# Performance work log

Hardware: AMD Instinct MI355X
Metric: run time of the kernel (lower is better)

Reference implementation:

```python
import jax, jax.numpy as jnp
import numpy as np

N_CH = 128      # n_channels (out_channels)
MID = 128       # mid_channels
NF = 16         # num_filters
N_NODES = 50000


def _omeg():
    i = jnp.arange(NF, dtype=jnp.float32)
    return (10.0 * N_CH ** (1.0 - 2.0 * i / NF)).reshape(1, NF)


def setup_inputs() -> dict:
    key = jax.random.key(0)
    ks = jax.random.split(key, 16)
    E = 800000
    inp = {
        "x": jax.random.normal(ks[0], (N_NODES, N_CH), jnp.float32),
        "edge_index": jax.random.randint(ks[1], (2, E), 0, N_NODES, jnp.int64),
        "edge_attr": jax.random.normal(ks[2], (E, N_CH), jnp.float32),
        "x_pos": jax.random.normal(ks[3], (N_NODES, 3), jnp.float32),
    }
    def lin(k, fan_in, fan_out):
        kw, kb = jax.random.split(k)
        bound = 1.0 / np.sqrt(fan_in)
        w = jax.random.uniform(kw, (fan_in, fan_out), jnp.float32, -bound, bound)
        b = jax.random.uniform(kb, (fan_out,), jnp.float32, -bound, bound)
        return w, b
    inp["w1"], inp["b1"] = lin(ks[4], N_CH, N_CH)          # atomwise1
    inp["mw1"], inp["mb1"] = lin(ks[5], 2 * NF + 2 * N_CH, MID)  # message MLP
    inp["mw2"], inp["mb2"] = lin(ks[6], MID, MID)
    inp["mw3"], inp["mb3"] = lin(ks[7], MID, N_CH)
    inp["w2"], inp["b2"] = lin(ks[8], N_CH, N_CH)          # atomwise2
    inp["w3"], inp["b3"] = lin(ks[9], N_CH, N_CH)          # atomwise3
    return inp


def reference(x, edge_index, edge_attr, x_pos, w1, b1, mw1, mb1, mw2, mb2, mw3, mb3, w2, b2, w3, b3):
    h = x @ w1 + b1                                   # atomwise1 [N, C]
    src, dst = edge_index[0], edge_index[1]           # PyG: x_j = src, x_i = dst
    r = jnp.linalg.norm(x_pos[dst] - x_pos[src], axis=-1, keepdims=True)  # [E,1], p=2
    feat = r * _omeg()                                # [E, NF]
    msg_in = jnp.concatenate([jnp.sin(feat), jnp.cos(feat), edge_attr, h[src]], axis=-1)
    m = jax.nn.gelu(msg_in @ mw1 + mb1, approximate=False)
    m = jax.nn.gelu(m @ mw2 + mb2, approximate=False)
    m = m @ mw3 + mb3                                 # dropout is identity at eval
    agg = jax.ops.segment_sum(m, dst, num_segments=N_NODES)
    h = h + agg                                       # residual in cfconv
    out = jax.nn.relu(h @ w2 + b2) @ w3 + b3
    return out
```

## Files before the change

### kernel.cpp

```cpp
#include <hip/hip_runtime.h>
#include <math.h>

#define NCH 128
#define TE 64
#define TF 32
#define AP 296
#define AF 132
#define WP 40
#define XP 136

typedef __attribute__((ext_vector_type(8))) _Float16 half8;
typedef __attribute__((ext_vector_type(4))) _Float16 half4;
typedef __attribute__((ext_vector_type(4))) float f32x4;

__device__ __forceinline__ float gelu_exact(float v) {
    return 0.5f * v * (1.0f + erff(v * 0.70710678118654752f));
}

__device__ __forceinline__ float erf_fast(float x) {
    float ax = fabsf(x);
    float t  = __builtin_amdgcn_rcpf(fmaf(0.3275911f, ax, 1.0f));
    float p  = fmaf(t, 1.061405429f, -1.453152027f);
    p = fmaf(t, p, 1.421413741f);
    p = fmaf(t, p, -0.284496736f);
    p = fmaf(t, p, 0.254829592f);
    float e  = exp2f(-ax * ax * 1.4426950408889634f);
    float r  = fmaf(-p * t, e, 1.0f);
    return copysignf(r, x);
}

__device__ __forceinline__ float gelu_fast(float v) {
    return 0.5f * v * (1.0f + erf_fast(v * 0.70710678118654752f));
}

__device__ __forceinline__ void sincos_rev(float rev, float* s, float* c) {
    float fr = rev - floorf(rev);
#if __has_builtin(__builtin_amdgcn_sinf) && __has_builtin(__builtin_amdgcn_cosf)
    *s = __builtin_amdgcn_sinf(fr);
    *c = __builtin_amdgcn_cosf(fr);
#else
    float rad = fr * 6.283185307179586f;
    *s = sinf(rad);
    *c = cosf(rad);
#endif
}

__global__ __launch_bounds__(256) void k_hist(const int* __restrict__ ei,
                                              int* __restrict__ cnt, int E) {
    int e = blockIdx.x * 256 + threadIdx.x;
    if (e < E) atomicAdd(&cnt[ei[E + e]], 1);
}

__global__ __launch_bounds__(256) void k_scan_local(const int* __restrict__ cnt,
                                                    int* __restrict__ fill,
                                                    int* __restrict__ bsum, int n) {
    __shared__ int sdata[256];
    const int tid = threadIdx.x;
    const int i = blockIdx.x * 256 + tid;
    int v = (i < n) ? cnt[i] : 0;
    sdata[tid] = v;
    __syncthreads();
    #pragma unroll
    for (int off = 1; off < 256; off <<= 1) {
        int t = (tid >= off) ? sdata[tid - off] : 0;
        __syncthreads();
        sdata[tid] += t;
        __syncthreads();
    }
    if (i < n) fill[i] = sdata[tid] - v;
    if (tid == 255) bsum[blockIdx.x] = sdata[255];
}

__global__ __launch_bounds__(256) void k_scan_bsum(int* __restrict__ bsum, int nb) {
    __shared__ int sdata[256];
    const int tid = threadIdx.x;
    int v = (tid < nb) ? bsum[tid] : 0;
    sdata[tid] = v;
    __syncthreads();
    #pragma unroll
    for (int off = 1; off < 256; off <<= 1) {
        int t = (tid >= off) ? sdata[tid - off] : 0;
        __syncthreads();
        sdata[tid] += t;
        __syncthreads();
    }
    if (tid < nb) bsum[tid] = sdata[tid] - v;
}

__global__ __launch_bounds__(256) void k_scan_add(int* __restrict__ fill,
                                                  const int* __restrict__ bsum, int n) {
    int i = blockIdx.x * 256 + threadIdx.x;
    if (i < n) fill[i] += bsum[blockIdx.x];
}

__global__ __launch_bounds__(256) void k_scan_serial(const int* __restrict__ cnt,
                                                     int* __restrict__ fill, int n) {
    __shared__ int sdata[256];
    __shared__ int carry;
    const int tid = threadIdx.x;
    if (tid == 0) carry = 0;
    __syncthreads();
    for (int base = 0; base < n; base += 256) {
        int i = base + tid;
        int v = (i < n) ? cnt[i] : 0;
        sdata[tid] = v;
        __syncthreads();
        #pragma unroll
        for (int off = 1; off < 256; off <<= 1) {
            int t = (tid >= off) ? sdata[tid - off] : 0;
            __syncthreads();
            sdata[tid] += t;
            __syncthreads();
        }
        int incl = sdata[tid];
        if (i < n) fill[i] = incl - v + carry;
        __syncthreads();
        if (tid == 255) carry += incl;
        __syncthreads();
    }
}

__global__ __launch_bounds__(256) void k_permute(const int* __restrict__ ei,
                                                 int* __restrict__ fill,
                                                 int* __restrict__ perm, int E) {
    int e = blockIdx.x * 256 + threadIdx.x;
    if (e < E) {
        int d = ei[E + e];
        int slot = atomicAdd(&fill[d], 1);
        perm[slot] = e;
    }
}

__global__ __launch_bounds__(256) void k_prep(const float* __restrict__ W,
                                              _Float16* __restrict__ out, int total) {
    int idx = blockIdx.x * 256 + threadIdx.x;
    if (idx >= total) return;
    int k = idx >> 7, n = idx & 127;
    out[(size_t)(k >> 5) * 4096 + n * 32 + (k & 31)] = (_Float16)W[idx];
}

__global__ __launch_bounds__(256) void k_prep_frag(const float* __restrict__ W,
                                                   _Float16* __restrict__ out,
                                                   int nchunks) {
    int idx = blockIdx.x * 256 + threadIdx.x;
    if (idx >= nchunks * 512) return;
    int c    = idx >> 9;
    int r    = idx & 511;
    int wv   = r >> 7;
    int nf   = (r >> 6) & 1;
    int lane = r & 63;
    int n  = wv * 32 + nf * 16 + (lane & 15);
    int k0 = c * 32 + (lane >> 4) * 8;
    half8 v;
    #pragma unroll
    for (int j = 0; j < 8; ++j) v[j] = (_Float16)W[(size_t)(k0 + j) * NCH + n];
    *(half8*)(out + (size_t)idx * 8) = v;
}

__global__ __launch_bounds__(256, 4) void k_aw1_mfma(
    const float* __restrict__ x, const _Float16* __restrict__ wc,
    const float* __restrict__ b1, float* __restrict__ h,
    _Float16* __restrict__ h2, int N)
{
    __shared__ __align__(16) _Float16 Xs[64][XP];
    __shared__ __align__(16) _Float16 Ws[128][WP];

    const int tid  = threadIdx.x;
    const int row0 = blockIdx.x * 64;
    const int lane = tid & 63;
    const int w    = tid >> 6;
    const int lrow = lane & 15;
    const int lk8  = lane >> 4;
    const int n0   = w * 32;

    const uint4* wsrc = (const uint4*)wc;
    uint4 pv0 = wsrc[tid], pv1 = wsrc[tid + 256];

    #pragma unroll
    for (int t = 0; t < 8; ++t) {
        int idx = tid + t * 256;
        int r = idx >> 5, f4 = idx & 31;
        int gr = row0 + r;
        float4 v = {0.f, 0.f, 0.f, 0.f};
        if (gr < N) v = *(const float4*)(x + (size_t)gr * NCH + f4 * 4);
        half4 p = {(_Float16)v.x, (_Float16)v.y, (_Float16)v.z, (_Float16)v.w};
        *(half4*)&Xs[r][f4 * 4] = p;
    }
    *(uint4*)&Ws[tid >> 2][(tid & 3) * 8]        = pv0;
    *(uint4*)&Ws[64 + (tid >> 2)][(tid & 3) * 8] = pv1;
    __syncthreads();

    f32x4 acc[4][2];
    #pragma unroll
    for (int mb = 0; mb < 4; ++mb)
        #pragma unroll
        for (int nf = 0; nf < 2; ++nf) acc[mb][nf] = (f32x4){0.f, 0.f, 0.f, 0.f};

    for (int i = 0; i < 4; ++i) {
        if (i < 3) {
            const uint4* s = (const uint4*)(wc + (i + 1) * 4096);
            pv0 = s[tid]; pv1 = s[tid + 256];
        }
        half8 av[4], bv[2];
        #pragma unroll
        for (int mb = 0; mb < 4; ++mb)
            av[mb] = *(const half8*)&Xs[mb * 16 + lrow][i * 32 + lk8 * 8];
        #pragma unroll
        for (int nf = 0; nf < 2; ++nf)
            bv[nf] = *(const half8*)&Ws[n0 + nf * 16 + lrow][lk8 * 8];
        #pragma unroll
        for (int mb = 0; mb < 4; ++mb)
            #pragma unroll
            for (int nf = 0; nf < 2; ++nf)
                acc[mb][nf] = __builtin_amdgcn_mfma_f32_16x16x32_f16(
                    av[mb], bv[nf], acc[mb][nf], 0, 0, 0);
        __syncthreads();
        if (i < 3) {
            *(uint4*)&Ws[tid >> 2][(tid & 3) * 8]        = pv0;
            *(uint4*)&Ws[64 + (tid >> 2)][(tid & 3) * 8] = pv1;
        }
        __syncthreads();
    }

    float bi0 = b1[n0 + lrow], bi1 = b1[n0 + 16 + lrow];
    #pragma unroll
    for (int mb = 0; mb < 4; ++mb)
        #pragma unroll
        for (int q = 0; q < 4; ++q) {
            int gr = row0 + mb * 16 + lk8 * 4 + q;
            if (gr < N) {
                float v0 = acc[mb][0][q] + bi0;
                float v1 = acc[mb][1][q] + bi1;
                h[(size_t)gr * NCH + n0 + lrow]       = v0;
                h[(size_t)gr * NCH + n0 + 16 + lrow]  = v1;
                h2[(size_t)gr * NCH + n0 + lrow]      = (_Float16)v0;
                h2[(size_t)gr * NCH + n0 + 16 + lrow] = (_Float16)v1;
            }
        }
}

__global__ __launch_bounds__(256, 8) void k_edges_mfma(
    const int* __restrict__ ei, const float* __restrict__ eattr,
    const float* __restrict__ xpos, const _Float16* __restrict__ h2,
    float* h,
    const int* __restrict__ perm,
    const _Float16* __restrict__ wf,
    const float* __restrict__ mb1, const float* __restrict__ mb2,
    const float* __restrict__ mb3, int E)
{
    __shared__ __align__(16) _Float16 As[TF][AP];
    __shared__ int permS[TF], dstS[TF];

    const int tid  = threadIdx.x;
    const int e0   = blockIdx.x * TF;
    const int lane = tid & 63;
    const int w    = tid >> 6;
    const int lrow = lane & 15;
    const int lk8  = lane >> 4;
    const int n0   = w * 32;

    const half8* bp = (const half8*)wf + (w * 128 + lane);

    half8 b[2][2];
    b[0][0] = bp[0];         b[0][1] = bp[64];
    b[1][0] = bp[512];       b[1][1] = bp[512 + 64];

    if (tid < TF) {
        int ge = e0 + tid;
        int pe = (ge < E) ? perm[ge] : -1;
        permS[tid] = pe;
        dstS[tid]  = (pe >= 0) ? ei[E + pe] : -1;
    }
    __syncthreads();

    float4 ea[4];
    #pragma unroll
    for (int t = 0; t < 4; ++t) {
        int idx = tid + t * 256;
        int pe = permS[idx >> 5];
        ea[t] = (pe >= 0) ? *(const float4*)(eattr + (size_t)pe * NCH + (idx & 31) * 4)
                          : (float4){0.f, 0.f, 0.f, 0.f};
    }
    uint4 hv[2];
    #pragma unroll
    for (int t = 0; t < 2; ++t) {
        int idx = tid + t * 256;
        int pe = permS[idx >> 4];
        int s = (pe >= 0) ? ei[pe] : 0;
        hv[t] = *(const uint4*)(h2 + (size_t)s * NCH + (idx & 15) * 8);
    }

    {
        int le = tid >> 3, i0 = tid & 7;
        int pe = permS[le];
        float r = 0.f;
        if (pe >= 0) {
            int s = ei[pe], d = dstS[le];
            float dx = xpos[d * 3 + 0] - xpos[s * 3 + 0];
            float dy = xpos[d * 3 + 1] - xpos[s * 3 + 1];
            float dz = xpos[d * 3 + 2] - xpos[s * 3 + 2];
            r = sqrtf(dx * dx + dy * dy + dz * dz);
        }
        #pragma unroll
        for (int u = 0; u < 2; ++u) {
            int i = i0 + u * 8;
            float omr = 1.5915494309f * exp2f(7.0f - 0.875f * (float)i);
            float sv, cv;
            sincos_rev(r * omr, &sv, &cv);
            As[le][i]      = (_Float16)sv;
            As[le][16 + i] = (_Float16)cv;
        }
    }
    #pragma unroll
    for (int t = 0; t < 4; ++t) {
        int idx = tid + t * 256;
        half4 p = {(_Float16)ea[t].x, (_Float16)ea[t].y,
                   (_Float16)ea[t].z, (_Float16)ea[t].w};
        *(half4*)&As[idx >> 5][32 + (idx & 31) * 4] = p;
    }
    #pragma unroll
    for (int t = 0; t < 2; ++t) {
        int idx = tid + t * 256;
        *(uint4*)&As[idx >> 4][160 + (idx & 15) * 8] = hv[t];
    }
    __syncthreads();

    f32x4 acc[2][2];
    #pragma unroll
    for (int mb = 0; mb < 2; ++mb)
        #pragma unroll
        for (int nf = 0; nf < 2; ++nf) acc[mb][nf] = (f32x4){0.f, 0.f, 0.f, 0.f};

    auto epi = [&](const float* __restrict__ mbv) {
        float bi0 = mbv[n0 + lrow], bi1 = mbv[n0 + 16 + lrow];
        #pragma unroll
        for (int mb = 0; mb < 2; ++mb)
            #pragma unroll
            for (int nf = 0; nf < 2; ++nf) {
                float bb = nf ? bi1 : bi0;
                #pragma unroll
                for (int q = 0; q < 4; ++q) {
                    float g = gelu_fast(acc[mb][nf][q] + bb);
                    As[mb * 16 + lk8 * 4 + q][n0 + nf * 16 + lrow] = (_Float16)g;
                }
                acc[mb][nf] = (f32x4){0.f, 0.f, 0.f, 0.f};
            }
    };

    #pragma unroll
    for (int i = 0; i < 17; ++i) {
        const int s  = i & 1;
        const int lc = (i < 9) ? i : (i < 13) ? (i - 9) : (i - 13);
        half8 av0 = *(const half8*)&As[lrow][lc * 32 + lk8 * 8];
        half8 av1 = *(const half8*)&As[16 + lrow][lc * 32 + lk8 * 8];
        __builtin_amdgcn_s_setprio(1);
        acc[0][0] = __builtin_amdgcn_mfma_f32_16x16x32_f16(av0, b[s][0], acc[0][0], 0, 0, 0);
        acc[0][1] = __builtin_amdgcn_mfma_f32_16x16x32_f16(av0, b[s][1], acc[0][1], 0, 0, 0);
        acc[1][0] = __builtin_amdgcn_mfma_f32_16x16x32_f16(av1, b[s][0], acc[1][0], 0, 0, 0);
        acc[1][1] = __builtin_amdgcn_mfma_f32_16x16x32_f16(av1, b[s][1], acc[1][1], 0, 0, 0);
        __builtin_amdgcn_s_setprio(0);
        if (i + 2 < 17) {
            b[s][0] = bp[(size_t)(i + 2) * 512];
            b[s][1] = bp[(size_t)(i + 2) * 512 + 64];
        }
        if (i == 8)  { __syncthreads(); epi(mb1); __syncthreads(); }
        if (i == 12) { __syncthreads(); epi(mb2); __syncthreads(); }
    }

    {
        float bi0 = mb3[n0 + lrow], bi1 = mb3[n0 + 16 + lrow];
        __syncthreads();
        float* Asf = (float*)&As[0][0];
        #pragma unroll
        for (int mb = 0; mb < 2; ++mb)
            #pragma unroll
            for (int nf = 0; nf < 2; ++nf) {
                float bb = nf ? bi1 : bi0;
                #pragma unroll
                for (int q = 0; q < 4; ++q) {
                    int e = mb * 16 + lk8 * 4 + q;
                    Asf[e * AF + n0 + nf * 16 + lrow] = acc[mb][nf][q] + bb;
                }
            }
        __syncthreads();

        const int c     = tid & 127;
        const int ebase = (tid >> 7) * 16;
        float run = 0.f;
        int prev = -1;
        #pragma unroll
        for (int le = 0; le < 16; ++le) {
            int d = dstS[ebase + le];
            float v = Asf[(ebase + le) * AF + c];
            if (d != prev) {
                if (prev >= 0) atomicAdd(h + (size_t)prev * NCH + c, run);
                run = 0.f;
                prev = d;
            }
            if (d >= 0) run += v;
        }
        if (prev >= 0) atomicAdd(h + (size_t)prev * NCH + c, run);
    }
}

__global__ __launch_bounds__(256, 4) void k_out_mfma(
    const float* h, const _Float16* __restrict__ w2c,
    const float* __restrict__ b2, const _Float16* __restrict__ w3c,
    const float* __restrict__ b3, float* out, int N)
{
    __shared__ __align__(16) _Float16 Xs[64][XP];
    __shared__ __align__(16) _Float16 Ws[128][WP];

    const int tid  = threadIdx.x;
    const int row0 = blockIdx.x * 64;
    const int lane = tid & 63;
    const int w    = tid >> 6;
    const int lrow = lane & 15;
    const int lk8  = lane >> 4;
    const int n0   = w * 32;

    const uint4* wsrc = (const uint4*)w2c;
    uint4 pv0 = wsrc[tid], pv1 = wsrc[tid + 256];

    #pragma unroll
    for (int t = 0; t < 8; ++t) {
        int idx = tid + t * 256;
        int r = idx >> 5, f4 = idx & 31;
        int gr = row0 + r;
        float4 v = {0.f, 0.f, 0.f, 0.f};
        if (gr < N) v = *(const float4*)(h + (size_t)gr * NCH + f4 * 4);
        half4 p = {(_Float16)v.x, (_Float16)v.y, (_Float16)v.z, (_Float16)v.w};
        *(half4*)&Xs[r][f4 * 4] = p;
    }
    *(uint4*)&Ws[tid >> 2][(tid & 3) * 8]        = pv0;
    *(uint4*)&Ws[64 + (tid >> 2)][(tid & 3) * 8] = pv1;
    __syncthreads();

    f32x4 acc[4][2];
    #pragma unroll
    for (int mb = 0; mb < 4; ++mb)
        #pragma unroll
        for (int nf = 0; nf < 2; ++nf) acc[mb][nf] = (f32x4){0.f, 0.f, 0.f, 0.f};

    for (int i = 0; i < 8; ++i) {
        if (i < 7) {
            int j = i + 1;
            const _Float16* nw = (j < 4) ? (w2c + j * 4096) : (w3c + (j - 4) * 4096);
            const uint4* s = (const uint4*)nw;
            pv0 = s[tid]; pv1 = s[tid + 256];
        }
        const int lc = i & 3;
        half8 av[4], bv[2];
        #pragma unroll
        for (int mb = 0; mb < 4; ++mb)
            av[mb] = *(const half8*)&Xs[mb * 16 + lrow][lc * 32 + lk8 * 8];
        #pragma unroll
        for (int nf = 0; nf < 2; ++nf)
            bv[nf] = *(const half8*)&Ws[n0 + nf * 16 + lrow][lk8 * 8];
        #pragma unroll
        for (int mb = 0; mb < 4; ++mb)
            #pragma unroll
            for (int nf = 0; nf < 2; ++nf)
                acc[mb][nf] = __builtin_amdgcn_mfma_f32_16x16x32_f16(
                    av[mb], bv[nf], acc[mb][nf], 0, 0, 0);

        __syncthreads();
        if (i == 3) {
            float bi0 = b2[n0 + lrow], bi1 = b2[n0 + 16 + lrow];
            #pragma unroll
            for (int mb = 0; mb < 4; ++mb)
                #pragma unroll
                for (int nf = 0; nf < 2; ++nf) {
                    float bb = nf ? bi1 : bi0;
                    #pragma unroll
                    for (int q = 0; q < 4; ++q) {
                        float g = fmaxf(acc[mb][nf][q] + bb, 0.f);
                        Xs[mb * 16 + lk8 * 4 + q][n0 + nf * 16 + lrow] = (_Float16)g;
                    }
                    acc[mb][nf] = (f32x4){0.f, 0.f, 0.f, 0.f};
                }
        }
        if (i < 7) {
            *(uint4*)&Ws[tid >> 2][(tid & 3) * 8]        = pv0;
            *(uint4*)&Ws[64 + (tid >> 2)][(tid & 3) * 8] = pv1;
        }
        __syncthreads();
    }

    float bi0 = b3[n0 + lrow], bi1 = b3[n0 + 16 + lrow];
    #pragma unroll
    for (int mb = 0; mb < 4; ++mb)
        #pragma unroll
        for (int q = 0; q < 4; ++q) {
            int gr = row0 + mb * 16 + lk8 * 4 + q;
            if (gr < N) {
                out[(size_t)gr * NCH + n0 + lrow]      = acc[mb][0][q] + bi0;
                out[(size_t)gr * NCH + n0 + 16 + lrow] = acc[mb][1][q] + bi1;
            }
        }
}

__global__ __launch_bounds__(256) void k_atomwise1(
    const float* __restrict__ x, const float* __restrict__ w1,
    const float* __restrict__ b1, float* __restrict__ h,
    float* __restrict__ h2, int N)
{
    __shared__ float xs[16][NCH];
    const int row0 = blockIdx.x * 16;
    const int tid = threadIdx.x;
    #pragma unroll
    for (int t = 0; t < 8; ++t) {
        int idx = tid + t * 256;
        int r = idx >> 7, c = idx & 127;
        int gr = row0 + r;
        xs[r][c] = (gr < N) ? x[(size_t)gr * NCH + c] : 0.f;
    }
    __syncthreads();
    const int j = tid & 127;
    const int rg = tid >> 7;
    float acc[8];
    #pragma unroll
    for (int i = 0; i < 8; ++i) acc[i] = 0.f;
    for (int k = 0; k < NCH; ++k) {
        float wv = w1[(size_t)k * NCH + j];
        #pragma unroll
        for (int i = 0; i < 8; ++i)
            acc[i] = fmaf(xs[rg * 8 + i][k], wv, acc[i]);
    }
    float bv = b1[j];
    #pragma unroll
    for (int i = 0; i < 8; ++i) {
        int gr = row0 + rg * 8 + i;
        if (gr < N) {
            float v = acc[i] + bv;
            h[(size_t)gr * NCH + j]  = v;
            h2[(size_t)gr * NCH + j] = v;
        }
    }
}

__global__ __launch_bounds__(256) void k_edges_f32(
    const int* __restrict__ ei, const float* __restrict__ eattr,
    const float* __restrict__ xpos, const float* __restrict__ h,
    const float* __restrict__ mw1, const float* __restrict__ mb1,
    const float* __restrict__ mw2, const float* __restrict__ mb2,
    const float* __restrict__ mw3, const float* __restrict__ mb3,
    float* __restrict__ agg, int E)
{
    __shared__ __align__(16) float Asf[TE][292];
    __shared__ float Wsf[32][NCH];
    __shared__ int srcS[TE];
    __shared__ int dstS[TE];
    const int tid = threadIdx.x;
    const int e0 = blockIdx.x * TE;
    if (tid < TE) {
        int e = e0 + tid;
        int s = 0, d = -1;
        float r = 0.f;
        if (e < E) {
            s = ei[e]; d = ei[E + e];
            float dx = xpos[d * 3 + 0] - xpos[s * 3 + 0];
            float dy = xpos[d * 3 + 1] - xpos[s * 3 + 1];
            float dz = xpos[d * 3 + 2] - xpos[s * 3 + 2];
            r = sqrtf(dx * dx + dy * dy + dz * dz);
        }
        srcS[tid] = s; dstS[tid] = d;
        #pragma unroll
        for (int i = 0; i < 16; ++i) {
            float om = 10.f * exp2f(7.0f - 0.875f * (float)i);
            float f = r * om;
            Asf[tid][i] = sinf(f); Asf[tid][16 + i] = cosf(f);
        }
    }
    __syncthreads();
    {
        const int half = tid >> 7;
        const int c = tid & 127;
        for (int ee = 0; ee < TE; ee += 2) {
            int le = ee + half;
            int e = e0 + le;
            if (e < E) {
                Asf[le][32 + c]  = eattr[(size_t)e * NCH + c];
                Asf[le][160 + c] = h[(size_t)srcS[le] * NCH + c];
            } else { Asf[le][32 + c] = 0.f; Asf[le][160 + c] = 0.f; }
        }
    }
    const int jl = tid & 31;
    const int g  = tid >> 5;
    float acc[8][4];
    auto run_layer = [&](const float* __restrict__ Wg, int K) {
        #pragma unroll
        for (int i = 0; i < 8; ++i)
            #pragma unroll
            for (int c = 0; c < 4; ++c) acc[i][c] = 0.f;
        for (int k0 = 0; k0 < K; k0 += 32) {
            __syncthreads();
            #pragma unroll
            for (int t = 0; t < 16; ++t) {
                int idx = tid + t * 256;
                Wsf[idx >> 7][idx & 127] =
                    Wg[(size_t)(k0 + (idx >> 7)) * NCH + (idx & 127)];
            }
            __syncthreads();
            #pragma unroll
            for (int kk = 0; kk < 32; kk += 4) {
                float4 a[8];
                #pragma unroll
                for (int i = 0; i < 8; ++i)
                    a[i] = *reinterpret_cast<const float4*>(&Asf[g * 8 + i][k0 + kk]);
                #pragma unroll
                for (int u = 0; u < 4; ++u) {
                    float w0 = Wsf[kk + u][jl];
                    float w1v = Wsf[kk + u][jl + 32];
                    float w2v = Wsf[kk + u][jl + 64];
                    float w3v = Wsf[kk + u][jl + 96];
                    #pragma unroll
                    for (int i = 0; i < 8; ++i) {
                        float avv = (&a[i].x)[u];
                        acc[i][0] = fmaf(avv, w0, acc[i][0]);
                        acc[i][1] = fmaf(avv, w1v, acc[i][1]);
                        acc[i][2] = fmaf(avv, w2v, acc[i][2]);
                        acc[i][3] = fmaf(avv, w3v, acc[i][3]);
                    }
                }
            }
        }
    };
    run_layer(mw1, 288);
    #pragma unroll
    for (int i = 0; i < 8; ++i)
        #pragma unroll
        for (int c = 0; c < 4; ++c) {
            int j = jl + 32 * c;
            Asf[g * 8 + i][j] = gelu_exact(acc[i][c] + mb1[j]);
        }
    run_layer(mw2, 128);
    #pragma unroll
    for (int i = 0; i < 8; ++i)
        #pragma unroll
        for (int c = 0; c < 4; ++c) {
            int j = jl + 32 * c;
            Asf[g * 8 + i][j] = gelu_exact(acc[i][c] + mb2[j]);
        }
    run_layer(mw3, 128);
    #pragma unroll
    for (int i = 0; i < 8; ++i) {
        int d = dstS[g * 8 + i];
        if (d >= 0) {
            #pragma unroll
            for (int c = 0; c < 4; ++c) {
                int j = jl + 32 * c;
                atomicAdd(&agg[(size_t)d * NCH + j], acc[i][c] + mb3[j]);
            }
        }
    }
}

__global__ __launch_bounds__(256) void k_out(
    const float* h, const float* aggOpt,
    const float* __restrict__ w2, const float* __restrict__ b2,
    const float* __restrict__ w3, const float* __restrict__ b3,
    float* out, int N)
{
    __shared__ float hs[16][NCH];
    __shared__ float ts[16][NCH];
    const int row0 = blockIdx.x * 16;
    const int tid = threadIdx.x;
    #pragma unroll
    for (int t = 0; t < 8; ++t) {
        int idx = tid + t * 256;
        int r = idx >> 7, c = idx & 127;
        int gr = row0 + r;
        float v = 0.f;
        if (gr < N) {
            v = h[(size_t)gr * NCH + c];
            if (aggOpt) v += aggOpt[(size_t)gr * NCH + c];
        }
        hs[r][c] = v;
    }
    __syncthreads();
    const int j = tid & 127;
    const int rg = tid >> 7;
    float acc[8];
    #pragma unroll
    for (int i = 0; i < 8; ++i) acc[i] = 0.f;
    for (int k = 0; k < NCH; ++k) {
        float wv = w2[(size_t)k * NCH + j];
        #pragma unroll
        for (int i = 0; i < 8; ++i)
            acc[i] = fmaf(hs[rg * 8 + i][k], wv, acc[i]);
    }
    float bv = b2[j];
    #pragma unroll
    for (int i = 0; i < 8; ++i)
        ts[rg * 8 + i][j] = fmaxf(acc[i] + bv, 0.f);
    __syncthreads();
    float acc2[8];
    #pragma unroll
    for (int i = 0; i < 8; ++i) acc2[i] = 0.f;
    for (int k = 0; k < NCH; ++k) {
        float wv = w3[(size_t)k * NCH + j];
        #pragma unroll
        for (int i = 0; i < 8; ++i)
            acc2[i] = fmaf(ts[rg * 8 + i][k], wv, acc2[i]);
    }
    float b3v = b3[j];
    #pragma unroll
    for (int i = 0; i < 8; ++i) {
        int gr = row0 + rg * 8 + i;
        if (gr < N) out[(size_t)gr * NCH + j] = acc2[i] + b3v;
    }
}

extern "C" void kernel_launch(void* const* d_in, const int* in_sizes, int n_in,
                              void* d_out, int out_size, void* d_ws, size_t ws_size,
                              hipStream_t stream)
{
    const float* x     = (const float*)d_in[0];
    const int*   ei    = (const int*)d_in[1];
    const float* eattr = (const float*)d_in[2];
    const float* xpos  = (const float*)d_in[3];
    const float* w1    = (const float*)d_in[4];
    const float* b1    = (const float*)d_in[5];
    const float* mw1   = (const float*)d_in[6];
    const float* mb1   = (const float*)d_in[7];
    const float* mw2   = (const float*)d_in[8];
    const float* mb2   = (const float*)d_in[9];
    const float* mw3   = (const float*)d_in[10];
    const float* mb3   = (const float*)d_in[11];
    const float* w2    = (const float*)d_in[12];
    const float* b2    = (const float*)d_in[13];
    const float* w3    = (const float*)d_in[14];
    const float* b3    = (const float*)d_in[15];

    const int N = in_sizes[0] / NCH;
    const int E = in_sizes[1] / 2;

    float* h = (float*)d_out;

    const int nbscan = (N + 255) / 256;
    const size_t h2_bytes = (size_t)N * NCH * sizeof(_Float16);
    const size_t wchunks  = 17 + 4 + 4 + 4;
    const size_t wbytes   = wchunks * 4096 * sizeof(_Float16);
    const size_t csr_bytes = ((size_t)2 * N + E + nbscan) * sizeof(int);
    const bool fast = ws_size >= h2_bytes + wbytes + csr_bytes;

    if (fast) {
        _Float16* h2   = (_Float16*)d_ws;
        _Float16* wf   = (_Float16*)((char*)d_ws + h2_bytes);
        _Float16* aw1c = wf + 17 * 4096;
        _Float16* o2c  = aw1c + 4 * 4096;
        _Float16* o3c  = o2c + 4 * 4096;
        int* cnt  = (int*)(o3c + 4 * 4096);
        int* fill = cnt + N;
        int* perm = fill + N;
        int* bsum = perm + E;

        hipMemsetAsync(cnt, 0, (size_t)N * sizeof(int), stream);
        k_hist<<<(E + 255) / 256, 256, 0, stream>>>(ei, cnt, E);
        if (nbscan <= 256) {
            k_scan_local<<<nbscan, 256, 0, stream>>>(cnt, fill, bsum, N);
            k_scan_bsum<<<1, 256, 0, stream>>>(bsum, nbscan);
            k_scan_add<<<nbscan, 256, 0, stream>>>(fill, bsum, N);
        } else {
            k_scan_serial<<<1, 256, 0, stream>>>(cnt, fill, N);
        }
        k_permute<<<(E + 255) / 256, 256, 0, stream>>>(ei, fill, perm, E);

        k_prep_frag<<<18, 256, 0, stream>>>(mw1, wf, 9);
        k_prep_frag<<<8, 256, 0, stream>>>(mw2, wf + 9 * 4096, 4);
        k_prep_frag<<<8, 256, 0, stream>>>(mw3, wf + 13 * 4096, 4);
        k_prep<<<64, 256, 0, stream>>>(w1, aw1c, 128 * 128);
        k_prep<<<64, 256, 0, stream>>>(w2, o2c, 128 * 128);
        k_prep<<<64, 256, 0, stream>>>(w3, o3c, 128 * 128);
        const int nb = (N + 63) / 64;
        k_aw1_mfma<<<nb, 256, 0, stream>>>(x, aw1c, b1, h, h2, N);
        k_edges_mfma<<<(E + TF - 1) / TF, 256, 0, stream>>>(
            ei, eattr, xpos, h2, h, perm, wf, mb1, mb2, mb3, E);
        k_out_mfma<<<nb, 256, 0, stream>>>(h, o2c, b2, o3c, b3, (float*)d_out, N);
    } else {
        float* agg = (float*)d_ws;
        k_atomwise1<<<(N + 15) / 16, 256, 0, stream>>>(x, w1, b1, h, agg, N);
        hipMemsetAsync(agg, 0, (size_t)N * NCH * sizeof(float), stream);
        k_edges_f32<<<(E + TE - 1) / TE, 256, 0, stream>>>(
            ei, eattr, xpos, h, mw1, mb1, mw2, mb2, mw3, mb3, agg, E);
        k_out<<<(N + 15) / 16, 256, 0, stream>>>(h, agg, w2, b2, w3, b3,
                                                 (float*)d_out, N);
    }
}
```

Baseline: 419.2 us.

## Load node-GEMM weights as register fragments and merge weight prep kernels

The atomwise1 and output kernels now load pre-swizzled fp16 weight fragments straight from global memory into registers, double-buffered, in place of staging them through shared memory with two barriers per k-chunk. The six weight-prep launches are merged into one kernel that uses the fragment layout for every weight matrix. Float-to-half conversion now uses packed round-toward-zero conversion, and the destination index in the edge scatter is made wave-uniform with readfirstlane. The aim is fewer barriers, less LDS traffic and less launch overhead. In exchange the kernels use more registers, and rounding changes from nearest to toward zero.

```diff
diff --git a/kernel.cpp b/kernel.cpp
--- a/kernel.cpp
+++ b/kernel.cpp
@@ -6,7 +6,6 @@
 #define TF 32
 #define AP 296
 #define AF 132
-#define WP 40
 #define XP 136
 
 typedef __attribute__((ext_vector_type(8))) _Float16 half8;
@@ -33,6 +32,18 @@
     return 0.5f * v * (1.0f + erf_fast(v * 0.70710678118654752f));
 }
 
+__device__ __forceinline__ half4 cvt4(float4 v) {
+#if __has_builtin(__builtin_amdgcn_cvt_pkrtz)
+    auto a = __builtin_amdgcn_cvt_pkrtz(v.x, v.y);
+    auto b = __builtin_amdgcn_cvt_pkrtz(v.z, v.w);
+    half4 r;
+    r[0] = a[0]; r[1] = a[1]; r[2] = b[0]; r[3] = b[1];
+    return r;
+#else
+    return (half4){(_Float16)v.x, (_Float16)v.y, (_Float16)v.z, (_Float16)v.w};
+#endif
+}
+
 __device__ __forceinline__ void sincos_rev(float rev, float* s, float* c) {
     float fr = rev - floorf(rev);
 #if __has_builtin(__builtin_amdgcn_sinf) && __has_builtin(__builtin_amdgcn_cosf)
@@ -131,19 +142,23 @@
     }
 }
 
-__global__ __launch_bounds__(256) void k_prep(const float* __restrict__ W,
-                                              _Float16* __restrict__ out, int total) {
-    int idx = blockIdx.x * 256 + threadIdx.x;
-    if (idx >= total) return;
-    int k = idx >> 7, n = idx & 127;
-    out[(size_t)(k >> 5) * 4096 + n * 32 + (k & 31)] = (_Float16)W[idx];
-}
-
-__global__ __launch_bounds__(256) void k_prep_frag(const float* __restrict__ W,
-                                                   _Float16* __restrict__ out,
-                                                   int nchunks) {
-    int idx = blockIdx.x * 256 + threadIdx.x;
-    if (idx >= nchunks * 512) return;
+__global__ __launch_bounds__(256) void k_prep_all(
+    const float* __restrict__ mw1, const float* __restrict__ mw2,
+    const float* __restrict__ mw3, const float* __restrict__ w1,
+    const float* __restrict__ w2, const float* __restrict__ w3,
+    _Float16* __restrict__ wf, _Float16* __restrict__ awf,
+    _Float16* __restrict__ o2f, _Float16* __restrict__ o3f)
+{
+    int b = blockIdx.x;
+    const float* W; _Float16* out; int nch;
+    if      (b < 18) { W = mw1; out = wf;             nch = 9; }
+    else if (b < 26) { W = mw2; out = wf + 9 * 4096;  nch = 4; b -= 18; }
+    else if (b < 34) { W = mw3; out = wf + 13 * 4096; nch = 4; b -= 26; }
+    else if (b < 42) { W = w1;  out = awf;            nch = 4; b -= 34; }
+    else if (b < 50) { W = w2;  out = o2f;            nch = 4; b -= 42; }
+    else             { W = w3;  out = o3f;            nch = 4; b -= 50; }
+    int idx = b * 256 + threadIdx.x;
+    if (idx >= nch * 512) return;
     int c    = idx >> 9;
     int r    = idx & 511;
     int wv   = r >> 7;
@@ -158,12 +173,11 @@
 }
 
 __global__ __launch_bounds__(256, 4) void k_aw1_mfma(
-    const float* __restrict__ x, const _Float16* __restrict__ wc,
+    const float* __restrict__ x, const _Float16* __restrict__ awf,
     const float* __restrict__ b1, float* __restrict__ h,
     _Float16* __restrict__ h2, int N)
 {
     __shared__ __align__(16) _Float16 Xs[64][XP];
-    __shared__ __align__(16) _Float16 Ws[128][WP];
 
     const int tid  = threadIdx.x;
     const int row0 = blockIdx.x * 64;
@@ -173,8 +187,10 @@
     const int lk8  = lane >> 4;
     const int n0   = w * 32;
 
-    const uint4* wsrc = (const uint4*)wc;
-    uint4 pv0 = wsrc[tid], pv1 = wsrc[tid + 256];
+    const half8* bp = (const half8*)awf + (w * 128 + lane);
+    half8 b[2][2];
+    b[0][0] = bp[0];   b[0][1] = bp[64];
+    b[1][0] = bp[512]; b[1][1] = bp[512 + 64];
 
     #pragma unroll
     for (int t = 0; t < 8; ++t) {
@@ -183,11 +199,8 @@
         int gr = row0 + r;
         float4 v = {0.f, 0.f, 0.f, 0.f};
         if (gr < N) v = *(const float4*)(x + (size_t)gr * NCH + f4 * 4);
-        half4 p = {(_Float16)v.x, (_Float16)v.y, (_Float16)v.z, (_Float16)v.w};
-        *(half4*)&Xs[r][f4 * 4] = p;
-    }
-    *(uint4*)&Ws[tid >> 2][(tid & 3) * 8]        = pv0;
-    *(uint4*)&Ws[64 + (tid >> 2)][(tid & 3) * 8] = pv1;
+        *(half4*)&Xs[r][f4 * 4] = cvt4(v);
+    }
     __syncthreads();
 
     f32x4 acc[4][2];
@@ -196,30 +209,22 @@
         #pragma unroll
         for (int nf = 0; nf < 2; ++nf) acc[mb][nf] = (f32x4){0.f, 0.f, 0.f, 0.f};
 
+    #pragma unroll
     for (int i = 0; i < 4; ++i) {
-        if (i < 3) {
-            const uint4* s = (const uint4*)(wc + (i + 1) * 4096);
-            pv0 = s[tid]; pv1 = s[tid + 256];
-        }
-        half8 av[4], bv[2];
+        const int s = i & 1;
+        half8 av[4];
         #pragma unroll
         for (int mb = 0; mb < 4; ++mb)
             av[mb] = *(const half8*)&Xs[mb * 16 + lrow][i * 32 + lk8 * 8];
         #pragma unroll
-        for (int nf = 0; nf < 2; ++nf)
-            bv[nf] = *(const half8*)&Ws[n0 + nf * 16 + lrow][lk8 * 8];
-        #pragma unroll
-        for (int mb = 0; mb < 4; ++mb)
-            #pragma unroll
-            for (int nf = 0; nf < 2; ++nf)
-                acc[mb][nf] = __builtin_amdgcn_mfma_f32_16x16x32_f16(
-                    av[mb], bv[nf], acc[mb][nf], 0, 0, 0);
-        __syncthreads();
-        if (i < 3) {
-            *(uint4*)&Ws[tid >> 2][(tid & 3) * 8]        = pv0;
-            *(uint4*)&Ws[64 + (tid >> 2)][(tid & 3) * 8] = pv1;
-        }
-        __syncthreads();
+        for (int mb = 0; mb < 4; ++mb) {
+            acc[mb][0] = __builtin_amdgcn_mfma_f32_16x16x32_f16(av[mb], b[s][0], acc[mb][0], 0, 0, 0);
+            acc[mb][1] = __builtin_amdgcn_mfma_f32_16x16x32_f16(av[mb], b[s][1], acc[mb][1], 0, 0, 0);
+        }
+        if (i + 2 < 4) {
+            b[s][0] = bp[(size_t)(i + 2) * 512];
+            b[s][1] = bp[(size_t)(i + 2) * 512 + 64];
+        }
     }
 
     float bi0 = b1[n0 + lrow], bi1 = b1[n0 + 16 + lrow];
@@ -260,10 +265,9 @@
     const int n0   = w * 32;
 
     const half8* bp = (const half8*)wf + (w * 128 + lane);
-
     half8 b[2][2];
-    b[0][0] = bp[0];         b[0][1] = bp[64];
-    b[1][0] = bp[512];       b[1][1] = bp[512 + 64];
+    b[0][0] = bp[0];   b[0][1] = bp[64];
+    b[1][0] = bp[512]; b[1][1] = bp[512 + 64];
 
     if (tid < TF) {
         int ge = e0 + tid;
@@ -314,9 +318,7 @@
     #pragma unroll
     for (int t = 0; t < 4; ++t) {
         int idx = tid + t * 256;
-        half4 p = {(_Float16)ea[t].x, (_Float16)ea[t].y,
-                   (_Float16)ea[t].z, (_Float16)ea[t].w};
-        *(half4*)&As[idx >> 5][32 + (idx & 31) * 4] = p;
+        *(half4*)&As[idx >> 5][32 + (idx & 31) * 4] = cvt4(ea[t]);
     }
     #pragma unroll
     for (int t = 0; t < 2; ++t) {
@@ -390,7 +392,7 @@
         int prev = -1;
         #pragma unroll
         for (int le = 0; le < 16; ++le) {
-            int d = dstS[ebase + le];
+            int d = __builtin_amdgcn_readfirstlane(dstS[ebase + le]);
             float v = Asf[(ebase + le) * AF + c];
             if (d != prev) {
                 if (prev >= 0) atomicAdd(h + (size_t)prev * NCH + c, run);
@@ -404,12 +406,11 @@
 }
 
 __global__ __launch_bounds__(256, 4) void k_out_mfma(
-    const float* h, const _Float16* __restrict__ w2c,
-    const float* __restrict__ b2, const _Float16* __restrict__ w3c,
+    const float* h, const _Float16* __restrict__ o2f,
+    const float* __restrict__ b2, const _Float16* __restrict__ o3f,
     const float* __restrict__ b3, float* out, int N)
 {
     __shared__ __align__(16) _Float16 Xs[64][XP];
-    __shared__ __align__(16) _Float16 Ws[128][WP];
 
     const int tid  = threadIdx.x;
     const int row0 = blockIdx.x * 64;
@@ -419,8 +420,11 @@
     const int lk8  = lane >> 4;
     const int n0   = w * 32;
 
-    const uint4* wsrc = (const uint4*)w2c;
-    uint4 pv0 = wsrc[tid], pv1 = wsrc[tid + 256];
+    const half8* bp2 = (const half8*)o2f + (w * 128 + lane);
+    const half8* bp3 = (const half8*)o3f + (w * 128 + lane);
+    half8 b[2][2];
+    b[0][0] = bp2[0];   b[0][1] = bp2[64];
+    b[1][0] = bp2[512]; b[1][1] = bp2[512 + 64];
 
     #pragma unroll
     for (int t = 0; t < 8; ++t) {
@@ -429,11 +433,8 @@
         int gr = row0 + r;
         float4 v = {0.f, 0.f, 0.f, 0.f};
         if (gr < N) v = *(const float4*)(h + (size_t)gr * NCH + f4 * 4);
-        half4 p = {(_Float16)v.x, (_Float16)v.y, (_Float16)v.z, (_Float16)v.w};
-        *(half4*)&Xs[r][f4 * 4] = p;
-    }
-    *(uint4*)&Ws[tid >> 2][(tid & 3) * 8]        = pv0;
-    *(uint4*)&Ws[64 + (tid >> 2)][(tid & 3) * 8] = pv1;
+        *(half4*)&Xs[r][f4 * 4] = cvt4(v);
+    }
     __syncthreads();
 
     f32x4 acc[4][2];
@@ -442,49 +443,61 @@
         #pragma unroll
         for (int nf = 0; nf < 2; ++nf) acc[mb][nf] = (f32x4){0.f, 0.f, 0.f, 0.f};
 
-    for (int i = 0; i < 8; ++i) {
-        if (i < 7) {
-            int j = i + 1;
-            const _Float16* nw = (j < 4) ? (w2c + j * 4096) : (w3c + (j - 4) * 4096);
-            const uint4* s = (const uint4*)nw;
-            pv0 = s[tid]; pv1 = s[tid + 256];
-        }
-        const int lc = i & 3;
-        half8 av[4], bv[2];
+    #pragma unroll
+    for (int i = 0; i < 4; ++i) {
+        const int s = i & 1;
+        half8 av[4];
         #pragma unroll
         for (int mb = 0; mb < 4; ++mb)
-            av[mb] = *(const half8*)&Xs[mb * 16 + lrow][lc * 32 + lk8 * 8];
-        #pragma unroll
-        for (int nf = 0; nf < 2; ++nf)
-            bv[nf] = *(const half8*)&Ws[n0 + nf * 16 + lrow][lk8 * 8];
+            av[mb] = *(const half8*)&Xs[mb * 16 + lrow][i * 32 + lk8 * 8];
+        #pragma unroll
+        for (int mb = 0; mb < 4; ++mb) {
+            acc[mb][0] = __builtin_amdgcn_mfma_f32_16x16x32_f16(av[mb], b[s][0], acc[mb][0], 0, 0, 0);
+            acc[mb][1] = __builtin_amdgcn_mfma_f32_16x16x32_f16(av[mb], b[s][1], acc[mb][1], 0, 0, 0);
+        }
+        if (i + 2 < 4) {
+            b[s][0] = bp2[(size_t)(i + 2) * 512];
+            b[s][1] = bp2[(size_t)(i + 2) * 512 + 64];
+        } else {
+            b[s][0] = bp3[(size_t)(i - 2) * 512];
+            b[s][1] = bp3[(size_t)(i - 2) * 512 + 64];
+        }
+    }
+    __syncthreads();
+
+    {
+        float bi0 = b2[n0 + lrow], bi1 = b2[n0 + 16 + lrow];
         #pragma unroll
         for (int mb = 0; mb < 4; ++mb)
             #pragma unroll
-            for (int nf = 0; nf < 2; ++nf)
-                acc[mb][nf] = __builtin_amdgcn_mfma_f32_16x16x32_f16(
-                    av[mb], bv[nf], acc[mb][nf], 0, 0, 0);
-
-        __syncthreads();
-        if (i == 3) {
-            float bi0 = b2[n0 + lrow], bi1 = b2[n0 + 16 + lrow];
-            #pragma unroll
-            for (int mb = 0; mb < 4; ++mb)
+            for (int nf = 0; nf < 2; ++nf) {
+                float bb = nf ? bi1 : bi0;
                 #pragma unroll
-                for (int nf = 0; nf < 2; ++nf) {
-                    float bb = nf ? bi1 : bi0;
-                    #pragma unroll
-                    for (int q = 0; q < 4; ++q) {
-                        float g = fmaxf(acc[mb][nf][q] + bb, 0.f);
-                        Xs[mb * 16 + lk8 * 4 + q][n0 + nf * 16 + lrow] = (_Float16)g;
-                    }
-                    acc[mb][nf] = (f32x4){0.f, 0.f, 0.f, 0.f};
+                for (int q = 0; q < 4; ++q) {
+                    float g = fmaxf(acc[mb][nf][q] + bb, 0.f);
+                    Xs[mb * 16 + lk8 * 4 + q][n0 + nf * 16 + lrow] = (_Float16)g;
                 }
-        }
-        if (i < 7) {
-            *(uint4*)&Ws[tid >> 2][(tid & 3) * 8]        = pv0;
-            *(uint4*)&Ws[64 + (tid >> 2)][(tid & 3) * 8] = pv1;
-        }
-        __syncthreads();
+                acc[mb][nf] = (f32x4){0.f, 0.f, 0.f, 0.f};
+            }
+    }
+    __syncthreads();
+
+    #pragma unroll
+    for (int i = 0; i < 4; ++i) {
+        const int s = i & 1;
+        half8 av[4];
+        #pragma unroll
+        for (int mb = 0; mb < 4; ++mb)
+            av[mb] = *(const half8*)&Xs[mb * 16 + lrow][i * 32 + lk8 * 8];
+        #pragma unroll
+        for (int mb = 0; mb < 4; ++mb) {
+            acc[mb][0] = __builtin_amdgcn_mfma_f32_16x16x32_f16(av[mb], b[s][0], acc[mb][0], 0, 0, 0);
+            acc[mb][1] = __builtin_amdgcn_mfma_f32_16x16x32_f16(av[mb], b[s][1], acc[mb][1], 0, 0, 0);
+        }
+        if (i + 2 < 4) {
+            b[s][0] = bp3[(size_t)(i + 2) * 512];
+            b[s][1] = bp3[(size_t)(i + 2) * 512 + 64];
+        }
     }
 
     float bi0 = b3[n0 + lrow], bi1 = b3[n0 + 16 + lrow];
@@ -746,12 +759,12 @@
     const bool fast = ws_size >= h2_bytes + wbytes + csr_bytes;
 
     if (fast) {
-        _Float16* h2   = (_Float16*)d_ws;
-        _Float16* wf   = (_Float16*)((char*)d_ws + h2_bytes);
-        _Float16* aw1c = wf + 17 * 4096;
-        _Float16* o2c  = aw1c + 4 * 4096;
-        _Float16* o3c  = o2c + 4 * 4096;
-        int* cnt  = (int*)(o3c + 4 * 4096);
+        _Float16* h2  = (_Float16*)d_ws;
+        _Float16* wf  = (_Float16*)((char*)d_ws + h2_bytes);
+        _Float16* awf = wf + 17 * 4096;
+        _Float16* o2f = awf + 4 * 4096;
+        _Float16* o3f = o2f + 4 * 4096;
+        int* cnt  = (int*)(o3f + 4 * 4096);
         int* fill = cnt + N;
         int* perm = fill + N;
         int* bsum = perm + E;
@@ -767,17 +780,13 @@
         }
         k_permute<<<(E + 255) / 256, 256, 0, stream>>>(ei, fill, perm, E);
 
-        k_prep_frag<<<18, 256, 0, stream>>>(mw1, wf, 9);
-        k_prep_frag<<<8, 256, 0, stream>>>(mw2, wf + 9 * 4096, 4);
-        k_prep_frag<<<8, 256, 0, stream>>>(mw3, wf + 13 * 4096, 4);
-        k_prep<<<64, 256, 0, stream>>>(w1, aw1c, 128 * 128);
-        k_prep<<<64, 256, 0, stream>>>(w2, o2c, 128 * 128);
-        k_prep<<<64, 256, 0, stream>>>(w3, o3c, 128 * 128);
+        k_prep_all<<<58, 256, 0, stream>>>(mw1, mw2, mw3, w1, w2, w3,
+                                           wf, awf, o2f, o3f);
         const int nb = (N + 63) / 64;
-        k_aw1_mfma<<<nb, 256, 0, stream>>>(x, aw1c, b1, h, h2, N);
+        k_aw1_mfma<<<nb, 256, 0, stream>>>(x, awf, b1, h, h2, N);
         k_edges_mfma<<<(E + TF - 1) / TF, 256, 0, stream>>>(
             ei, eattr, xpos, h2, h, perm, wf, mb1, mb2, mb3, E);
-        k_out_mfma<<<nb, 256, 0, stream>>>(h, o2c, b2, o3c, b3, (float*)d_out, N);
+        k_out_mfma<<<nb, 256, 0, stream>>>(h, o2f, b2, o3f, b3, (float*)d_out, N);
     } else {
         float* agg = (float*)d_ws;
         k_atomwise1<<<(N + 15) / 16, 256, 0, stream>>>(x, w1, b1, h, agg, N);
```

Result: faster. 396.0 us (-5.5%).
